# Kernel tuning notes

Measured on AMD Instinct MI355X. Metric: run time of the kernel, lower is better.

Reference implementation:

```python
import jax, jax.numpy as jnp
import numpy as np

B, N, C = 8, 1025, 768  # batch, tokens (1 CLS + 32*32 patches), channels
H = 12                  # heads
D = C // H              # head dim = 64
EPS = 1e-6

def _rot(x):
    # stack([-x[..., 1::2], x[..., ::2]], -1).reshape(x.shape)
    return jnp.stack([-x[..., 1::2], x[..., ::2]], axis=-1).reshape(x.shape)

def apply_rot_embed_cat(x, emb):
    # emb: [N-1, 2*D] = concat(sin, cos); x: [B, H, N-1, D]
    sin, cos = jnp.split(emb, 2, axis=-1)
    return x * cos + _rot(x) * sin

def setup_inputs() -> dict:
    key = jax.random.key(0)
    ks = jax.random.split(key, 8)
    s = 0.02
    return {
        "x": jax.random.normal(ks[0], (B, N, C), jnp.float32),
        "rope": jax.random.normal(ks[1], (N - 1, 2 * D), jnp.float32),
        "w_qkv": jax.random.normal(ks[2], (C, 3 * C), jnp.float32) * s,
        "q_bias": jax.random.normal(ks[3], (C,), jnp.float32) * s,
        "v_bias": jax.random.normal(ks[4], (C,), jnp.float32) * s,
        "gamma": jnp.ones((C,), jnp.float32),
        "beta": jnp.zeros((C,), jnp.float32),
        "w_proj": jax.random.normal(ks[5], (C, C), jnp.float32) * s,
        "b_proj": jnp.zeros((C,), jnp.float32),
    }

def reference(x, rope, w_qkv, q_bias, v_bias, gamma, beta, w_proj, b_proj):
    scale = D ** (-0.5)
    qkv_bias = jnp.concatenate([q_bias, jnp.zeros_like(q_bias), v_bias], axis=0)
    qkv = x @ w_qkv + qkv_bias  # [B, N, 3C]
    qkv = qkv.reshape(B, N, 3, H, D).transpose(2, 0, 3, 1, 4)  # [3, B, H, N, D]
    q, k, v = qkv[0], qkv[1], qkv[2]
    # RoPE on non-CLS tokens only
    q = jnp.concatenate([q[:, :, :1], apply_rot_embed_cat(q[:, :, 1:], rope)], axis=2)
    k = jnp.concatenate([k[:, :, :1], apply_rot_embed_cat(k[:, :, 1:], rope)], axis=2)
    attn = jnp.einsum('bhqd,bhkd->bhqk', q * scale, k)
    attn = jax.nn.softmax(attn, axis=-1)
    y = jnp.einsum('bhqk,bhkd->bhqd', attn, v)
    y = y.transpose(0, 2, 1, 3).reshape(B, N, C)
    # LayerNorm
    mu = jnp.mean(y, axis=-1, keepdims=True)
    var = jnp.mean(jnp.square(y - mu), axis=-1, keepdims=True)
    y = (y - mu) * jax.lax.rsqrt(var + EPS) * gamma + beta
    return y @ w_proj + b_proj
```

## Files before the change

### kernel.cpp

```cpp
#include <hip/hip_runtime.h>

typedef __bf16 bf16_t;
typedef __bf16 bf16x8 __attribute__((ext_vector_type(8)));
typedef float f32x4 __attribute__((ext_vector_type(4)));
typedef float f32x16 __attribute__((ext_vector_type(16)));
typedef unsigned short u16;
typedef unsigned int u32;

#define NTOK 1025
#define MTOT 8200
#define MPAD 8448
#define CDIM 768

#define GLOAD(dst, p) \
  asm volatile("global_load_dwordx4 %0, %1, off" : "=&v"(dst) : "v"((const void*)(p)))

__device__ __forceinline__ u16 f2bf(float f) {
  union { float f; unsigned u; } v; v.f = f;
  unsigned r = v.u + 0x7fffu + ((v.u >> 16) & 1u);
  return (u16)(r >> 16);
}
__device__ __forceinline__ float bf2f(u16 h) {
  union { unsigned u; float f; } v; v.u = ((unsigned)h) << 16; return v.f;
}
__device__ __forceinline__ u32 cvtpk(float lo, float hi) {
  u32 r; asm("v_cvt_pk_bf16_f32 %0, %1, %2" : "=v"(r) : "v"(lo), "v"(hi)); return r;
}

__global__ __launch_bounds__(256) void conv_xf(const float4* __restrict__ x4,
                                               u16* __restrict__ xf) {
  __shared__ u16 tile[16][776];
  int mt = blockIdx.x;
  int t = threadIdx.x;
#pragma unroll
  for (int it = 0; it < 12; ++it) {
    int id = it * 256 + t;
    int r = id / 192, c4 = id % 192;
    int m = mt * 16 + r;
    if (m < MTOT) {
      float4 f = x4[(size_t)m * 192 + c4];
      ushort4 o; o.x = f2bf(f.x); o.y = f2bf(f.y); o.z = f2bf(f.z); o.w = f2bf(f.w);
      *(ushort4*)&tile[r][c4 * 4] = o;
    }
  }
  __syncthreads();
#pragma unroll
  for (int it = 0; it < 6; ++it) {
    int cid = it * 256 + t;
    int kt = cid >> 6, lane = cid & 63;
    uint4 w = *(const uint4*)&tile[lane & 15][kt * 32 + (lane >> 4) * 8];
    *(uint4*)&xf[(((size_t)mt * 24 + kt) * 64 + lane) * 8] = w;
  }
}

__global__ __launch_bounds__(64) void transp_wf(const float* __restrict__ in, int N,
                                                u16* __restrict__ wf) {
  __shared__ u16 lds[16][32];
  int n0 = blockIdx.x * 16, k0 = blockIdx.y * 32;
  int t = threadIdx.x;
#pragma unroll
  for (int it = 0; it < 8; ++it) {
    int e = it * 64 + t;
    int kk = e >> 4, nn = e & 15;
    lds[nn][kk] = f2bf(in[(size_t)(k0 + kk) * N + n0 + nn]);
  }
  __syncthreads();
  uint4 w = *(const uint4*)&lds[t & 15][(t >> 4) * 8];
  *(uint4*)&wf[((((size_t)(n0 >> 4)) * 24 + (k0 >> 5)) * 64 + t) * 8] = w;
}

template <bool TRANS>
__device__ __forceinline__ void fdloop(const u16* __restrict__ afr, const u16* __restrict__ bfr,
                                       int m0, int n0, int lane, int wr, int wc,
                                       f32x4 (*acc)[4]) {
  const u16* ab = afr + ((size_t)((m0 >> 4) + wr * 4) * 1536 + lane) * 8;
  const u16* bb = bfr + ((size_t)((n0 >> 4) + wc * 4) * 1536 + lane) * 8;
  bf16x8 S[3][8];
  auto LOADA = [&](int s, int kt) {
#pragma unroll
    for (int i = 0; i < 4; ++i)
      GLOAD(S[s][i], ab + (size_t)i * 12288 + (size_t)kt * 512);
#pragma unroll
    for (int j = 0; j < 4; ++j)
      GLOAD(S[s][4 + j], bb + (size_t)j * 12288 + (size_t)kt * 512);
  };
  auto COMP = [&](bf16x8 (&Sc)[8]) {
    __builtin_amdgcn_s_setprio(1);
#pragma unroll
    for (int x = 0; x < 4; ++x)
#pragma unroll
      for (int y = 0; y < 4; ++y)
        acc[x][y] = TRANS
            ? __builtin_amdgcn_mfma_f32_16x16x32_bf16(Sc[4 + x], Sc[y], acc[x][y], 0, 0, 0)
            : __builtin_amdgcn_mfma_f32_16x16x32_bf16(Sc[x], Sc[4 + y], acc[x][y], 0, 0, 0);
    __builtin_amdgcn_s_setprio(0);
  };
  LOADA(0, 0);
  LOADA(1, 1);
#pragma unroll
  for (int kt = 0; kt < 24; ++kt) {
    if (kt < 22) {
      LOADA((kt + 2) % 3, kt + 2);
      asm volatile("s_waitcnt vmcnt(16)");
    } else if (kt == 22) {
      asm volatile("s_waitcnt vmcnt(8)");
    } else {
      asm volatile("s_waitcnt vmcnt(0)");
    }
    __builtin_amdgcn_sched_barrier(0);
    COMP(S[kt % 3]);
  }
}

__global__ __launch_bounds__(256, 2) void qkv_gemm_all(
    const u16* __restrict__ xf, const u16* __restrict__ wf,
    const float* __restrict__ qbias, const float* __restrict__ vbias,
    const float* __restrict__ rope,
    u16* __restrict__ q, u16* __restrict__ kfr, u16* __restrict__ vfr) {
  const int NB = 18;
  int tau0 = blockIdx.x;
  int xcd = tau0 & 7, pos = tau0 >> 3;
  int tau = (xcd < 2) ? xcd * 147 + pos : 294 + (xcd - 2) * 146 + pos;
  int bx = tau % NB, by = tau / NB;
  int m0 = by * 128;
  int t = threadIdx.x;
  int lane = t & 63, wave = t >> 6;
  int ln = lane & 15, hi = lane >> 4;
  int wr = wave >> 1, wc = wave & 1;

  if (bx < 12) {
    int n0 = bx * 128;
    f32x4 acc[4][4] = {};
    fdloop<true>(xf, wf, m0, n0, lane, wr, wc, acc);

    const float scale = 0.125f * 1.4426950408889634f;
#pragma unroll
    for (int ii = 0; ii < 4; ++ii) {
      int m = m0 + wr * 64 + ii * 16 + ln;
      if (m < MTOT) {
        int b = m / NTOK;
        int n = m - b * NTOK;
        const float* rp = rope + (size_t)(n - 1) * 128;
#pragma unroll
        for (int jj = 0; jj < 4; ++jj) {
          int c4 = n0 + wc * 64 + jj * 16 + hi * 4;
          int part = (c4 >= CDIM) ? 1 : 0;
          int cc = c4 - part * CDIM;
          int h = cc >> 6, d4 = cc & 63;
          float v0 = acc[jj][ii][0], v1 = acc[jj][ii][1];
          float v2 = acc[jj][ii][2], v3 = acc[jj][ii][3];
          if (part == 0) {
            float4 qb = *(const float4*)(qbias + cc);
            v0 += qb.x; v1 += qb.y; v2 += qb.z; v3 += qb.w;
          }
          float o0, o1, o2, o3;
          if (n > 0) {
            float4 sn = *(const float4*)(rp + d4);
            float4 cs = *(const float4*)(rp + 64 + d4);
            o0 = v0 * cs.x - v1 * sn.x;
            o1 = v1 * cs.y + v0 * sn.y;
            o2 = v2 * cs.z - v3 * sn.z;
            o3 = v3 * cs.w + v2 * sn.w;
          } else { o0 = v0; o1 = v1; o2 = v2; o3 = v3; }
          uint2 w;
          if (part == 0) {
            w.x = cvtpk(o0 * scale, o1 * scale); w.y = cvtpk(o2 * scale, o3 * scale);
            *(uint2*)(q + ((size_t)(h * MPAD + m)) * 64 + d4) = w;
          } else {
            w.x = cvtpk(o0, o1); w.y = cvtpk(o2, o3);
            int kt2 = n >> 5, lqn = n & 31;
            int sF = d4 >> 4, h2d = (d4 >> 3) & 1, j0 = d4 & 7;
            u16* dst = kfr + ((((size_t)(h * 8 + b) * 34 + kt2) * 4 + sF) * 64
                              + h2d * 32 + lqn) * 8 + j0;
            *(uint2*)dst = w;
          }
        }
      }
    }
  } else {
    int n0 = 1536 + (bx - 12) * 128;
    f32x4 acc[4][4] = {};
    fdloop<false>(xf, wf, m0, n0, lane, wr, wc, acc);

#pragma unroll
    for (int i = 0; i < 4; ++i) {
      int mrow = m0 + wr * 64 + i * 16 + hi * 4;
#pragma unroll
      for (int j = 0; j < 4; ++j) {
        int cv = n0 - 1536 + wc * 64 + j * 16 + ln;
        int h = cv >> 6, d = cv & 63;
        int hf = d >> 5, lqd = d & 31;
        float vb = vbias[cv];
#pragma unroll
        for (int r = 0; r < 4; ++r) {
          int mr = mrow + r;
          if (mr < MTOT) {
            int b = mr / NTOK;
            int n = mr - b * NTOK;
            size_t idx = ((((size_t)(h * 8 + b) * 17 + (n >> 6)) * 4 + ((n >> 4) & 3)) * 2 + hf) * 512
                       + (size_t)((((n >> 3) & 1) * 32 + lqd) * 8 + (n & 7));
            vfr[idx] = f2bf(acc[i][j][r] + vb);
          }
        }
      }
    }
  }
}

template <bool PF, bool MASK>
__device__ __forceinline__ void flash_iter(
    bf16x8 (&kf)[8], bf16x8 (&kn)[8], int pftile, int it,
    const u16* kfb, const u16* vfb, int h2,
    const bf16x8 (&qf)[4], f32x16 (&acc)[2], float& l) {
  if (PF) {
    const u16* kp2 = kfb + (size_t)pftile * 4096;
#pragma unroll
    for (int c = 0; c < 2; ++c)
#pragma unroll
      for (int s = 0; s < 4; ++s)
        kn[c * 4 + s] = *(const bf16x8*)(kp2 + c * 2048 + s * 512);
  }
  bf16x8 vf[8];
  const u16* vp2 = vfb + (size_t)it * 4096;
#pragma unroll
  for (int hf = 0; hf < 2; ++hf)
#pragma unroll
    for (int s = 0; s < 4; ++s)
      vf[hf * 4 + s] = *(const bf16x8*)(vp2 + (s * 2 + hf) * 512);
  f32x16 sc[2] = {};
  __builtin_amdgcn_s_setprio(1);
#pragma unroll
  for (int c = 0; c < 2; ++c)
#pragma unroll
    for (int s = 0; s < 4; ++s)
      sc[c] = __builtin_amdgcn_mfma_f32_32x32x16_bf16(kf[c * 4 + s], qf[s], sc[c], 0, 0, 0);
  __builtin_amdgcn_s_setprio(0);
#pragma unroll
  for (int c = 0; c < 2; ++c)
#pragma unroll
    for (int r = 0; r < 16; ++r)
      sc[c][r] = __builtin_amdgcn_exp2f(sc[c][r]);
  if (MASK) {
#pragma unroll
    for (int c = 0; c < 2; ++c)
#pragma unroll
      for (int r = 0; r < 16; ++r) {
        int kk = it * 64 + c * 32 + (r & 3) + 8 * (r >> 2) + 4 * h2;
        if (kk >= NTOK) sc[c][r] = 0.f;
      }
  }
  float rs = 0.f;
#pragma unroll
  for (int c = 0; c < 2; ++c)
#pragma unroll
    for (int r = 0; r < 16; ++r) rs += sc[c][r];
  l += rs;
  bf16x8 frag[4];
#pragma unroll
  for (int c = 0; c < 2; ++c) {
    u32 k0 = cvtpk(sc[c][0], sc[c][1]),   k1 = cvtpk(sc[c][2], sc[c][3]);
    u32 k2 = cvtpk(sc[c][4], sc[c][5]),   k3 = cvtpk(sc[c][6], sc[c][7]);
    u32 k4 = cvtpk(sc[c][8], sc[c][9]),   k5 = cvtpk(sc[c][10], sc[c][11]);
    u32 k6 = cvtpk(sc[c][12], sc[c][13]), k7 = cvtpk(sc[c][14], sc[c][15]);
    asm("v_permlane32_swap_b32 %0, %1" : "+v"(k0), "+v"(k2));
    asm("v_permlane32_swap_b32 %0, %1" : "+v"(k1), "+v"(k3));
    asm("v_permlane32_swap_b32 %0, %1" : "+v"(k4), "+v"(k6));
    asm("v_permlane32_swap_b32 %0, %1" : "+v"(k5), "+v"(k7));
    union { u32 u[4]; bf16x8 v; } u0, u1;
    u0.u[0] = k0; u0.u[1] = k1; u0.u[2] = k2; u0.u[3] = k3;
    u1.u[0] = k4; u1.u[1] = k5; u1.u[2] = k6; u1.u[3] = k7;
    frag[c * 2] = u0.v; frag[c * 2 + 1] = u1.v;
  }
  __builtin_amdgcn_s_setprio(1);
#pragma unroll
  for (int hf = 0; hf < 2; ++hf)
#pragma unroll
    for (int s = 0; s < 4; ++s)
      acc[hf] = __builtin_amdgcn_mfma_f32_32x32x16_bf16(vf[hf * 4 + s], frag[s], acc[hf], 0, 0, 0);
  __builtin_amdgcn_s_setprio(0);
}

__global__ __launch_bounds__(256, 2) void flash_attn(
    const u16* __restrict__ q, const u16* __restrict__ kfr,
    const u16* __restrict__ vfr, u16* __restrict__ y) {
  int f = blockIdx.x;
  int xcd = f & 7, idx = f >> 3;
  int bh = xcd * 12 + idx / 9;
  int qt = idx - (idx / 9) * 9;
  int b = bh / 12, h = bh - b * 12;
  int t = threadIdx.x, lane = t & 63, w = t >> 6;
  int lq = lane & 31, h2 = lane >> 5;
  int q0 = qt * 128 + w * 32;
  if (q0 >= NTOK) return;
  int qrow = q0 + lq; if (qrow > NTOK - 1) qrow = NTOK - 1;

  const u16* qp = q + ((size_t)(h * MPAD) + (size_t)b * NTOK + qrow) * 64;
  bf16x8 qf[4];
#pragma unroll
  for (int s = 0; s < 4; ++s)
    qf[s] = *(const bf16x8*)&qp[s * 16 + h2 * 8];

  const u16* kfb = kfr + (size_t)(h * 8 + b) * 34 * 2048 + lane * 8;
  const u16* vfb = vfr + (size_t)(h * 8 + b) * 17 * 4096 + lane * 8;

  f32x16 acc[2] = {};
  float l = 0.f;

  bf16x8 ka[8], kb2[8];
#pragma unroll
  for (int c = 0; c < 2; ++c)
#pragma unroll
    for (int s = 0; s < 4; ++s)
      ka[c * 4 + s] = *(const bf16x8*)(kfb + c * 2048 + s * 512);

#pragma unroll 1
  for (int i2 = 0; i2 < 8; ++i2) {
    flash_iter<true, false>(ka, kb2, 2 * i2 + 1, 2 * i2, kfb, vfb, h2, qf, acc, l);
    flash_iter<true, false>(kb2, ka, 2 * i2 + 2, 2 * i2 + 1, kfb, vfb, h2, qf, acc, l);
  }
  flash_iter<false, true>(ka, kb2, 0, 16, kfb, vfb, h2, qf, acc, l);

  int row = q0 + lq;
  if (row < NTOK) {
    float lt = l + __shfl_xor(l, 32, 64);
    float inv = 1.f / lt;
    u16* yr = y + ((size_t)(b * NTOK + row)) * CDIM + h * 64;
#pragma unroll
    for (int hf = 0; hf < 2; ++hf)
#pragma unroll
      for (int g = 0; g < 4; ++g) {
        int d0 = hf * 32 + 8 * g + 4 * h2;
        ushort4 o;
        o.x = f2bf(acc[hf][g * 4 + 0] * inv);
        o.y = f2bf(acc[hf][g * 4 + 1] * inv);
        o.z = f2bf(acc[hf][g * 4 + 2] * inv);
        o.w = f2bf(acc[hf][g * 4 + 3] * inv);
        *(ushort4*)&yr[d0] = o;
      }
  }
}

__global__ __launch_bounds__(256) void lnorm(const u16* __restrict__ y,
                                             const float* __restrict__ gamma,
                                             const float* __restrict__ beta,
                                             u16* __restrict__ yf) {
  int row = blockIdx.x;
  const u16* yr = y + (size_t)row * CDIM;
  int t = threadIdx.x;
  float v[3];
  float s = 0.f, s2 = 0.f;
#pragma unroll
  for (int i = 0; i < 3; ++i) {
    v[i] = bf2f(yr[t + 256 * i]);
    s += v[i]; s2 += v[i] * v[i];
  }
#pragma unroll
  for (int msk = 1; msk < 64; msk <<= 1) {
    s  += __shfl_xor(s, msk, 64);
    s2 += __shfl_xor(s2, msk, 64);
  }
  __shared__ float ws[8];
  int w = t >> 6, lane = t & 63;
  if (lane == 0) { ws[w] = s; ws[4 + w] = s2; }
  __syncthreads();
  s = ws[0] + ws[1] + ws[2] + ws[3];
  s2 = ws[4] + ws[5] + ws[6] + ws[7];
  float mu = s * (1.f / 768.f);
  float var = s2 * (1.f / 768.f) - mu * mu;
  float rstd = rsqrtf(var + 1e-6f);
  if (t < 96) {
    union { uint4 u4; u16 u[8]; } iv, ov;
    iv.u4 = *(const uint4*)&yr[t * 8];
    const float* gp = gamma + t * 8;
    const float* bp = beta + t * 8;
#pragma unroll
    for (int j = 0; j < 8; ++j)
      ov.u[j] = f2bf((bf2f(iv.u[j]) - mu) * rstd * gp[j] + bp[j]);
    int kt = t >> 2, ln2 = (row & 15) + 16 * (t & 3), mt = row >> 4;
    *(uint4*)&yf[(((size_t)mt * 24 + kt) * 64 + ln2) * 8] = ov.u4;
  }
}

__global__ __launch_bounds__(256, 2) void proj_gemm(
    const u16* __restrict__ yf, const u16* __restrict__ wf,
    const float* __restrict__ bias, float* __restrict__ out) {
  const int NB = 6;
  int tau0 = blockIdx.x;
  int xcd = tau0 & 7, pos = tau0 >> 3;
  int tau = (xcd < 6) ? xcd * 49 + pos : 294 + (xcd - 6) * 48 + pos;
  int bx = tau % NB, by = tau / NB;
  int m0 = by * 128, n0 = bx * 128;
  int t = threadIdx.x;
  int lane = t & 63, wave = t >> 6;
  int ln = lane & 15, hi = lane >> 4;
  int wr = wave >> 1, wc = wave & 1;

  f32x4 acc[4][4] = {};
  fdloop<true>(yf, wf, m0, n0, lane, wr, wc, acc);

#pragma unroll
  for (int ii = 0; ii < 4; ++ii) {
    int m = m0 + wr * 64 + ii * 16 + ln;
    if (m < MTOT) {
      float* dr = out + (size_t)m * CDIM;
#pragma unroll
      for (int jj = 0; jj < 4; ++jj) {
        int c4 = n0 + wc * 64 + jj * 16 + hi * 4;
        float4 bv = *(const float4*)(bias + c4);
        float4 o;
        o.x = acc[jj][ii][0] + bv.x;
        o.y = acc[jj][ii][1] + bv.y;
        o.z = acc[jj][ii][2] + bv.z;
        o.w = acc[jj][ii][3] + bv.w;
        *(float4*)(dr + c4) = o;
      }
    }
  }
}

extern "C" void kernel_launch(void* const* d_in, const int* in_sizes, int n_in,
                              void* d_out, int out_size, void* d_ws, size_t ws_size,
                              hipStream_t stream) {
  const float* x      = (const float*)d_in[0];
  const float* rope   = (const float*)d_in[1];
  const float* w_qkv  = (const float*)d_in[2];
  const float* q_bias = (const float*)d_in[3];
  const float* v_bias = (const float*)d_in[4];
  const float* gamma  = (const float*)d_in[5];
  const float* beta   = (const float*)d_in[6];
  const float* w_proj = (const float*)d_in[7];
  const float* b_proj = (const float*)d_in[8];
  float* out = (float*)d_out;

  char* ws = (char*)d_ws;
  u16* xf   = (u16*)(ws);
  u16* ybf  = (u16*)(ws);
  u16* wfq  = (u16*)(ws + 12976128);
  u16* wfp  = (u16*)(ws + 16515072);
  u16* qbuf = (u16*)(ws + 17694720);
  u16* yf   = (u16*)(ws + 17694720);
  u16* kfr  = (u16*)(ws + 30670848);
  u16* vfr  = (u16*)(ws + 44040192);

  conv_xf<<<dim3(513), 256, 0, stream>>>((const float4*)x, xf);
  transp_wf<<<dim3(144, 24), 64, 0, stream>>>(w_qkv, 2304, wfq);
  transp_wf<<<dim3(48, 24), 64, 0, stream>>>(w_proj, 768, wfp);

  qkv_gemm_all<<<dim3(1170), 256, 0, stream>>>(xf, wfq, q_bias, v_bias, rope,
                                               qbuf, kfr, vfr);
  flash_attn<<<dim3(864), 256, 0, stream>>>(qbuf, kfr, vfr, ybf);
  lnorm<<<8200, 256, 0, stream>>>(ybf, gamma, beta, yf);
  proj_gemm<<<dim3(390), 256, 0, stream>>>(yf, wfp, b_proj, out);
}
```

Measured before the change: 159.7 us.

## Enlarge GEMM tiles to 256x128 with double-buffered register prefetch

Both the QKV and projection GEMMs move from 128x128 to 256x128 block tiles, with each wave computing a 128x64 sub-tile (8x4 MFMA accumulators). This roughly halves the grid size and raises the reuse of each loaded fragment. The register prefetch pipeline drops from triple to double buffering, with 12 fragments per stage, to fit the larger accumulator set. In exchange, register pressure is higher, which may lower occupancy or cause spills, and the smaller grid (594 and 198 blocks) leaves fewer waves to hide latency and may balance unevenly across CUs.

```diff
diff --git a/kernel.cpp b/kernel.cpp
--- a/kernel.cpp
+++ b/kernel.cpp
@@ -70,45 +70,42 @@
 }
 
 template <bool TRANS>
-__device__ __forceinline__ void fdloop(const u16* __restrict__ afr, const u16* __restrict__ bfr,
-                                       int m0, int n0, int lane, int wr, int wc,
-                                       f32x4 (*acc)[4]) {
-  const u16* ab = afr + ((size_t)((m0 >> 4) + wr * 4) * 1536 + lane) * 8;
-  const u16* bb = bfr + ((size_t)((n0 >> 4) + wc * 4) * 1536 + lane) * 8;
-  bf16x8 S[3][8];
+__device__ __forceinline__ void fdloop2(const u16* __restrict__ tfr, const u16* __restrict__ ffr,
+                                        int mt0, int nt0, int lane,
+                                        f32x4 (*acc)[4]) {
+  const u16* ab = tfr + ((size_t)mt0 * 1536 + lane) * 8;
+  const u16* bb = ffr + ((size_t)nt0 * 1536 + lane) * 8;
+  bf16x8 S[2][12];
   auto LOADA = [&](int s, int kt) {
 #pragma unroll
-    for (int i = 0; i < 4; ++i)
+    for (int i = 0; i < 8; ++i)
       GLOAD(S[s][i], ab + (size_t)i * 12288 + (size_t)kt * 512);
 #pragma unroll
     for (int j = 0; j < 4; ++j)
-      GLOAD(S[s][4 + j], bb + (size_t)j * 12288 + (size_t)kt * 512);
+      GLOAD(S[s][8 + j], bb + (size_t)j * 12288 + (size_t)kt * 512);
   };
-  auto COMP = [&](bf16x8 (&Sc)[8]) {
+  auto COMP = [&](bf16x8 (&Sc)[12]) {
     __builtin_amdgcn_s_setprio(1);
 #pragma unroll
-    for (int x = 0; x < 4; ++x)
+    for (int x = 0; x < 8; ++x)
 #pragma unroll
       for (int y = 0; y < 4; ++y)
         acc[x][y] = TRANS
-            ? __builtin_amdgcn_mfma_f32_16x16x32_bf16(Sc[4 + x], Sc[y], acc[x][y], 0, 0, 0)
-            : __builtin_amdgcn_mfma_f32_16x16x32_bf16(Sc[x], Sc[4 + y], acc[x][y], 0, 0, 0);
+            ? __builtin_amdgcn_mfma_f32_16x16x32_bf16(Sc[8 + y], Sc[x], acc[x][y], 0, 0, 0)
+            : __builtin_amdgcn_mfma_f32_16x16x32_bf16(Sc[x], Sc[8 + y], acc[x][y], 0, 0, 0);
     __builtin_amdgcn_s_setprio(0);
   };
   LOADA(0, 0);
-  LOADA(1, 1);
 #pragma unroll
   for (int kt = 0; kt < 24; ++kt) {
-    if (kt < 22) {
-      LOADA((kt + 2) % 3, kt + 2);
-      asm volatile("s_waitcnt vmcnt(16)");
-    } else if (kt == 22) {
-      asm volatile("s_waitcnt vmcnt(8)");
+    if (kt < 23) {
+      LOADA((kt + 1) & 1, kt + 1);
+      asm volatile("s_waitcnt vmcnt(12)");
     } else {
       asm volatile("s_waitcnt vmcnt(0)");
     }
     __builtin_amdgcn_sched_barrier(0);
-    COMP(S[kt % 3]);
+    COMP(S[kt & 1]);
   }
 }
 
@@ -120,9 +117,9 @@
   const int NB = 18;
   int tau0 = blockIdx.x;
   int xcd = tau0 & 7, pos = tau0 >> 3;
-  int tau = (xcd < 2) ? xcd * 147 + pos : 294 + (xcd - 2) * 146 + pos;
+  int tau = (xcd < 2) ? xcd * 75 + pos : 150 + (xcd - 2) * 74 + pos;
   int bx = tau % NB, by = tau / NB;
-  int m0 = by * 128;
+  int m0 = by * 256;
   int t = threadIdx.x;
   int lane = t & 63, wave = t >> 6;
   int ln = lane & 15, hi = lane >> 4;
@@ -130,13 +127,13 @@
 
   if (bx < 12) {
     int n0 = bx * 128;
-    f32x4 acc[4][4] = {};
-    fdloop<true>(xf, wf, m0, n0, lane, wr, wc, acc);
+    f32x4 acc[8][4] = {};
+    fdloop2<true>(xf, wf, (m0 >> 4) + wr * 8, (n0 >> 4) + wc * 4, lane, acc);
 
     const float scale = 0.125f * 1.4426950408889634f;
 #pragma unroll
-    for (int ii = 0; ii < 4; ++ii) {
-      int m = m0 + wr * 64 + ii * 16 + ln;
+    for (int ii = 0; ii < 8; ++ii) {
+      int m = m0 + wr * 128 + ii * 16 + ln;
       if (m < MTOT) {
         int b = m / NTOK;
         int n = m - b * NTOK;
@@ -147,8 +144,8 @@
           int part = (c4 >= CDIM) ? 1 : 0;
           int cc = c4 - part * CDIM;
           int h = cc >> 6, d4 = cc & 63;
-          float v0 = acc[jj][ii][0], v1 = acc[jj][ii][1];
-          float v2 = acc[jj][ii][2], v3 = acc[jj][ii][3];
+          float v0 = acc[ii][jj][0], v1 = acc[ii][jj][1];
+          float v2 = acc[ii][jj][2], v3 = acc[ii][jj][3];
           if (part == 0) {
             float4 qb = *(const float4*)(qbias + cc);
             v0 += qb.x; v1 += qb.y; v2 += qb.z; v3 += qb.w;
@@ -179,12 +176,12 @@
     }
   } else {
     int n0 = 1536 + (bx - 12) * 128;
-    f32x4 acc[4][4] = {};
-    fdloop<false>(xf, wf, m0, n0, lane, wr, wc, acc);
-
-#pragma unroll
-    for (int i = 0; i < 4; ++i) {
-      int mrow = m0 + wr * 64 + i * 16 + hi * 4;
+    f32x4 acc[8][4] = {};
+    fdloop2<false>(xf, wf, (m0 >> 4) + wr * 8, (n0 >> 4) + wc * 4, lane, acc);
+
+#pragma unroll
+    for (int i = 0; i < 8; ++i) {
+      int mrow = m0 + wr * 128 + i * 16 + hi * 4;
 #pragma unroll
       for (int j = 0; j < 4; ++j) {
         int cv = n0 - 1536 + wc * 64 + j * 16 + ln;
@@ -387,20 +384,20 @@
   const int NB = 6;
   int tau0 = blockIdx.x;
   int xcd = tau0 & 7, pos = tau0 >> 3;
-  int tau = (xcd < 6) ? xcd * 49 + pos : 294 + (xcd - 6) * 48 + pos;
+  int tau = (xcd < 6) ? xcd * 25 + pos : 150 + (xcd - 6) * 24 + pos;
   int bx = tau % NB, by = tau / NB;
-  int m0 = by * 128, n0 = bx * 128;
+  int m0 = by * 256, n0 = bx * 128;
   int t = threadIdx.x;
   int lane = t & 63, wave = t >> 6;
   int ln = lane & 15, hi = lane >> 4;
   int wr = wave >> 1, wc = wave & 1;
 
-  f32x4 acc[4][4] = {};
-  fdloop<true>(yf, wf, m0, n0, lane, wr, wc, acc);
-
-#pragma unroll
-  for (int ii = 0; ii < 4; ++ii) {
-    int m = m0 + wr * 64 + ii * 16 + ln;
+  f32x4 acc[8][4] = {};
+  fdloop2<true>(yf, wf, (m0 >> 4) + wr * 8, (n0 >> 4) + wc * 4, lane, acc);
+
+#pragma unroll
+  for (int ii = 0; ii < 8; ++ii) {
+    int m = m0 + wr * 128 + ii * 16 + ln;
     if (m < MTOT) {
       float* dr = out + (size_t)m * CDIM;
 #pragma unroll
@@ -408,10 +405,10 @@
         int c4 = n0 + wc * 64 + jj * 16 + hi * 4;
         float4 bv = *(const float4*)(bias + c4);
         float4 o;
-        o.x = acc[jj][ii][0] + bv.x;
-        o.y = acc[jj][ii][1] + bv.y;
-        o.z = acc[jj][ii][2] + bv.z;
-        o.w = acc[jj][ii][3] + bv.w;
+        o.x = acc[ii][jj][0] + bv.x;
+        o.y = acc[ii][jj][1] + bv.y;
+        o.z = acc[ii][jj][2] + bv.z;
+        o.w = acc[ii][jj][3] + bv.w;
         *(float4*)(dr + c4) = o;
       }
     }
@@ -446,9 +443,9 @@
   transp_wf<<<dim3(144, 24), 64, 0, stream>>>(w_qkv, 2304, wfq);
   transp_wf<<<dim3(48, 24), 64, 0, stream>>>(w_proj, 768, wfp);
 
-  qkv_gemm_all<<<dim3(1170), 256, 0, stream>>>(xf, wfq, q_bias, v_bias, rope,
-                                               qbuf, kfr, vfr);
+  qkv_gemm_all<<<dim3(594), 256, 0, stream>>>(xf, wfq, q_bias, v_bias, rope,
+                                              qbuf, kfr, vfr);
   flash_attn<<<dim3(864), 256, 0, stream>>>(qbuf, kfr, vfr, ybf);
   lnorm<<<8200, 256, 0, stream>>>(ybf, gamma, beta, yf);
-  proj_gemm<<<dim3(390), 256, 0, stream>>>(yf, wfp, b_proj, out);
-}
+  proj_gemm<<<dim3(198), 256, 0, stream>>>(yf, wfp, b_proj, out);
+}
```

Result: no change. 160.9 us (+0.8%).
